# Optimization experiments

Hardware: AMD Instinct MI355X
Metric: run time of the kernel (lower is better)

The kernel has to match this reference:

```python
import jax, jax.numpy as jnp
import numpy as np

B, T, D, H = 4, 1024, 1024, 16


def setup_inputs() -> dict:
    key = jax.random.key(0)
    ks = jax.random.split(key, 8)
    s = 0.02
    return {
        "query": jax.random.normal(ks[0], (B, T, D), jnp.float32),
        "key": jax.random.normal(ks[1], (B, T, D), jnp.float32),
        "values": jax.random.normal(ks[2], (B, T, D), jnp.float32),
        "Wq": jax.random.normal(ks[3], (D, D), jnp.float32) * s,
        "bq": jnp.zeros((D,), jnp.float32),
        "Wv": jax.random.normal(ks[4], (D, D), jnp.float32) * s,
        "bv": jnp.zeros((D,), jnp.float32),
        "Wo": jax.random.normal(ks[5], (D, D), jnp.float32) * s,
        "bo": jnp.zeros((D,), jnp.float32),
        "gammas": jax.random.normal(ks[6], (H,), jnp.float32) * 0.1,
        "ln_g": jnp.ones((D,), jnp.float32),
        "ln_b": jnp.zeros((D,), jnp.float32),
    }


def _layer(query, key, values, Wq, bq, Wv, bv, Wo, bo, gammas, ln_g, ln_b):
    b, t, d = query.shape
    h = gammas.shape[0]
    dk = d // h

    def proj(x, W, bias):  # torch Linear: x @ W.T + b, then split heads -> (b,h,t,dk)
        y = jnp.einsum('btd,ed->bte', x, W) + bias
        return y.reshape(b, t, h, dk).transpose(0, 2, 1, 3)

    q = proj(query, Wq, bq)
    k = proj(key, Wq, bq)   # kq_same=True
    v = proj(values, Wv, bv)

    scores = jnp.einsum('bhqd,bhkd->bhqk', q, k) / np.float32(np.sqrt(dk))
    idx = jnp.arange(t)
    pos = jnp.abs(idx[:, None] - idx[None, :]).astype(scores.dtype)  # |i-j|, (t,t)
    mask = idx[:, None] > idx[None, :]  # strict lower tril (peek_cur=False)
    neg = jnp.asarray(-1e32, scores.dtype)

    # gamma time-effect (computed without grad in original)
    s_ = jax.nn.softmax(jnp.where(mask, scores, neg), axis=-1)
    distcum = jnp.cumsum(s_, axis=-1)
    disttotal = jnp.sum(s_, axis=-1, keepdims=True)
    dist = jnp.sqrt(jnp.clip((disttotal - distcum) * pos, 0.0, None))
    dist = jax.lax.stop_gradient(dist)
    gamma_eff = -jnp.abs(gammas)[None, :, None, None]  # (1,h,1,1)
    total_effect = jnp.clip(jnp.exp(dist * gamma_eff), 1e-5, 1e5)
    scores = scores * total_effect

    p = jax.nn.softmax(jnp.where(mask, scores, neg), axis=-1)
    p = jnp.where(mask, p, 0.0)
    # maxout rescale (maxout=True since peek_cur=False)
    scale = jnp.minimum(1.0 / jnp.max(p, axis=-1, keepdims=True), 5.0)
    p = p * scale

    out = jnp.einsum('bhqk,bhkd->bhqd', p, v)
    concat = out.transpose(0, 2, 1, 3).reshape(b, t, d)
    attn_out = jnp.einsum('btd,ed->bte', concat, Wo) + bo

    x = query + attn_out  # residual (dropout is identity in eval)
    mu = jnp.mean(x, axis=-1, keepdims=True)
    var = jnp.var(x, axis=-1, keepdims=True)
    return (x - mu) / jnp.sqrt(var + 1e-5) * ln_g + ln_b


def reference(query, key, values, Wq, bq, Wv, bv, Wo, bo, gammas, ln_g, ln_b):
    return _layer(query, key, values, Wq, bq, Wv, bv, Wo, bo, gammas, ln_g, ln_b)
```

## Files before the change

kernel.cpp:

```cpp
#include <hip/hip_runtime.h>
#include <hip/hip_bf16.h>
#include <stdint.h>


typedef unsigned short ushort_t;
typedef __attribute__((ext_vector_type(8))) short short8;
typedef __attribute__((ext_vector_type(8))) unsigned short u16x8;
typedef __attribute__((ext_vector_type(4))) float f32x4;
typedef __attribute__((ext_vector_type(4))) unsigned short u16x4;

#define GLB_CAST(p) ((const __attribute__((address_space(1))) void*)(p))
#define LDS_CAST(p) ((__attribute__((address_space(3))) void*)(p))

#if __has_builtin(__builtin_amdgcn_exp2f)
#define EXP2F(x) __builtin_amdgcn_exp2f(x)
#else
#define EXP2F(x) exp2f(x)
#endif

#define LOG2E 1.44269504f

__device__ __forceinline__ float b2f(ushort_t u) {
  union { unsigned int i; float f; } x; x.i = ((unsigned int)u) << 16; return x.f;
}
__device__ __forceinline__ ushort_t f2b(float f) {
  __hip_bfloat16 h = __float2bfloat16(f);
  return *reinterpret_cast<ushort_t*>(&h);
}
__device__ __forceinline__ float wave_sum(float v) {
  #pragma unroll
  for (int d = 32; d > 0; d >>= 1) v += __shfl_xor(v, d);
  return v;
}

__global__ void conv6_f32_bf16(const float* __restrict__ s0, const float* __restrict__ s1,
                               const float* __restrict__ s2, const float* __restrict__ s3,
                               const float* __restrict__ s4, const float* __restrict__ s5,
                               ushort_t* __restrict__ d0, ushort_t* __restrict__ d1,
                               ushort_t* __restrict__ d2, ushort_t* __restrict__ d3,
                               ushort_t* __restrict__ d4, ushort_t* __restrict__ d5,
                               int n4tok, int n4w) {
  const int y = blockIdx.y;
  const float* srcs[6] = {s0, s1, s2, s3, s4, s5};
  ushort_t*    dsts[6] = {d0, d1, d2, d3, d4, d5};
  const int n4 = (y < 3) ? n4tok : n4w;
  int i = blockIdx.x * blockDim.x + threadIdx.x;
  if (i < n4) {
    const float4 v = reinterpret_cast<const float4*>(srcs[y])[i];
    u16x4 o;
    o[0] = f2b(v.x); o[1] = f2b(v.y); o[2] = f2b(v.z); o[3] = f2b(v.w);
    reinterpret_cast<u16x4*>(dsts[y])[i] = o;
  }
}

__device__ __forceinline__ void gemm_core(const ushort_t* __restrict__ A,
                                          const ushort_t* __restrict__ Bt,
                                          int m0, int n0,
                                          ushort_t* As, ushort_t* Bs,
                                          f32x4 (&acc)[4][4]) {
  const int tid = threadIdx.x, lane = tid & 63;
  const int wid = tid >> 6;
  const int wr = (wid >> 1) * 64, wc = (wid & 1) * 64;
  for (int k0 = 0; k0 < 1024; k0 += 32) {
    #pragma unroll
    for (int it = 0; it < 2; ++it) {
      const int idx = tid * 8 + it * 2048;
      const int r = idx >> 5, kk = idx & 31;
      __builtin_amdgcn_global_load_lds(GLB_CAST(&A[(size_t)(m0 + r) * 1024 + k0 + kk]),
                                       LDS_CAST(&As[idx]), 16, 0, 0);
      __builtin_amdgcn_global_load_lds(GLB_CAST(&Bt[(size_t)(n0 + r) * 1024 + k0 + kk]),
                                       LDS_CAST(&Bs[idx]), 16, 0, 0);
    }
    __syncthreads();
    short8 af[4], bfv[4];
    #pragma unroll
    for (int m = 0; m < 4; ++m)
      af[m] = *reinterpret_cast<const short8*>(&As[(wr + m * 16 + (lane & 15)) * 32 + (lane >> 4) * 8]);
    #pragma unroll
    for (int n = 0; n < 4; ++n)
      bfv[n] = *reinterpret_cast<const short8*>(&Bs[(wc + n * 16 + (lane & 15)) * 32 + (lane >> 4) * 8]);
    #pragma unroll
    for (int m = 0; m < 4; ++m)
      #pragma unroll
      for (int n = 0; n < 4; ++n)
        acc[m][n] = __builtin_amdgcn_mfma_f32_16x16x32_bf16(af[m], bfv[n], acc[m][n], 0, 0, 0);
    __syncthreads();
  }
}

__global__ __launch_bounds__(256) void gemm_proj(
    const ushort_t* __restrict__ qb, const ushort_t* __restrict__ kb, const ushort_t* __restrict__ vb,
    const ushort_t* __restrict__ Wqb, const ushort_t* __restrict__ Wvb,
    const float* __restrict__ bq, const float* __restrict__ bvv,
    ushort_t* __restrict__ Qh, ushort_t* __restrict__ Kh, ushort_t* __restrict__ Vt) {
  __shared__ ushort_t As[128 * 32], Bs[128 * 32];
  const ushort_t* A; const ushort_t* Bt; const float* bias;
  if (blockIdx.z == 0)      { A = qb; Bt = Wqb; bias = bq;  }
  else if (blockIdx.z == 1) { A = kb; Bt = Wqb; bias = bq;  }
  else                      { A = vb; Bt = Wvb; bias = bvv; }
  const int m0 = blockIdx.y * 128, n0 = blockIdx.x * 128;
  f32x4 zero = {0.f, 0.f, 0.f, 0.f};
  f32x4 acc[4][4];
  #pragma unroll
  for (int m = 0; m < 4; ++m)
    #pragma unroll
    for (int n = 0; n < 4; ++n) acc[m][n] = zero;
  gemm_core(A, Bt, m0, n0, As, Bs, acc);
  const int lane = threadIdx.x & 63, wid = threadIdx.x >> 6;
  const int wr = (wid >> 1) * 64, wc = (wid & 1) * 64;
  if (blockIdx.z == 2) {
    #pragma unroll
    for (int m = 0; m < 4; ++m)
      #pragma unroll
      for (int n = 0; n < 4; ++n) {
        const int rowb = m0 + wr + m * 16 + (lane >> 4) * 4;
        const int col  = n0 + wc + n * 16 + (lane & 15);
        u16x4 pk;
        #pragma unroll
        for (int r4 = 0; r4 < 4; ++r4) pk[r4] = f2b(acc[m][n][r4] + bias[col]);
        const int bi = rowb >> 10, t = rowb & 1023;
        *reinterpret_cast<u16x4*>(
            &Vt[((size_t)(bi * 16 + (col >> 6)) * 64 + (col & 63)) * 1024 + t]) = pk;
      }
  } else {
    ushort_t* dst = (blockIdx.z == 0) ? Qh : Kh;
    #pragma unroll
    for (int m = 0; m < 4; ++m)
      #pragma unroll
      for (int n = 0; n < 4; ++n)
        #pragma unroll
        for (int r4 = 0; r4 < 4; ++r4) {
          const int row = m0 + wr + m * 16 + (lane >> 4) * 4 + r4;
          const int col = n0 + wc + n * 16 + (lane & 15);
          const float v = acc[m][n][r4] + bias[col];
          const int bi = row >> 10, t = row & 1023, h = col >> 6, dd = col & 63;
          dst[((size_t)(bi * 16 + h) * 1024 + t) * 64 + dd] = f2b(v);
        }
  }
}

__global__ __launch_bounds__(256) void gemm_out(
    const ushort_t* __restrict__ A, const ushort_t* __restrict__ Bt,
    const float* __restrict__ bias, const float* __restrict__ resid,
    float* __restrict__ dstF) {
  __shared__ ushort_t As[128 * 32], Bs[128 * 32];
  const int m0 = blockIdx.y * 128, n0 = blockIdx.x * 128;
  f32x4 zero = {0.f, 0.f, 0.f, 0.f};
  f32x4 acc[4][4];
  #pragma unroll
  for (int m = 0; m < 4; ++m)
    #pragma unroll
    for (int n = 0; n < 4; ++n) acc[m][n] = zero;
  gemm_core(A, Bt, m0, n0, As, Bs, acc);
  const int lane = threadIdx.x & 63, wid = threadIdx.x >> 6;
  const int wr = (wid >> 1) * 64, wc = (wid & 1) * 64;
  #pragma unroll
  for (int m = 0; m < 4; ++m)
    #pragma unroll
    for (int n = 0; n < 4; ++n)
      #pragma unroll
      for (int r4 = 0; r4 < 4; ++r4) {
        const int row = m0 + wr + m * 16 + (lane >> 4) * 4 + r4;
        const int col = n0 + wc + n * 16 + (lane & 15);
        const size_t o = (size_t)row * 1024 + col;
        dstF[o] = acc[m][n][r4] + bias[col] + resid[o];
      }
}

template<int CH>
__device__ __forceinline__ void phase_b(ushort_t* __restrict__ Sb, const int i0,
                                        const int w, const int lane, const float gamx) {
  const int c0 = CH * lane;
  int idxA = 0, idxB = 0;
  if constexpr (CH == 16) {
    const int ca = 2 * lane, cb = 2 * lane + 1;
    idxA = (ca ^ ((ca >> 3) & 7)) << 3;
    idxB = (cb ^ ((cb >> 3) & 7)) << 3;
  } else {
    const int c = c0 >> 3;
    idxA = ((c ^ ((c >> 3) & 7)) << 3) + (c0 & 7);
  }
  for (int rr = 0; rr < 4; ++rr) {
    const int r = w * 4 + rr;
    const int i = i0 + r;
    ushort_t* __restrict__ Row = &Sb[r * 1032];
    if (i == 0) {
      #pragma unroll
      for (int e = 0; e < CH; ++e) {
        if constexpr (CH == 16) Row[(e < 8) ? (idxA + e) : (idxB + e - 8)] = 0;
        else                    Row[idxA + e] = 0;
      }
      continue;
    }
    float s[CH];
    if constexpr (CH == 16) {
      const u16x8 ra = *reinterpret_cast<const u16x8*>(&Row[idxA]);
      const u16x8 rb = *reinterpret_cast<const u16x8*>(&Row[idxB]);
      #pragma unroll
      for (int e = 0; e < 8; ++e) { s[e] = b2f(ra[e]); s[8 + e] = b2f(rb[e]); }
    } else if constexpr (CH == 8) {
      const u16x8 ra = *reinterpret_cast<const u16x8*>(&Row[idxA]);
      #pragma unroll
      for (int e = 0; e < 8; ++e) s[e] = b2f(ra[e]);
    } else if constexpr (CH == 4) {
      const u16x4 ra = *reinterpret_cast<const u16x4*>(&Row[idxA]);
      #pragma unroll
      for (int e = 0; e < 4; ++e) s[e] = b2f(ra[e]);
    } else if constexpr (CH == 2) {
      s[0] = b2f(Row[idxA]); s[1] = b2f(Row[idxA + 1]);
    } else {
      s[0] = b2f(Row[idxA]);
    }
    const int nact = min(max(i - c0, 0), CH);
    float run = 0.f;
    #pragma unroll
    for (int e = 0; e < CH; ++e) {
      s[e] = (e < nact) ? s[e] * LOG2E : -__builtin_inff();
      run += EXP2F(s[e]);
    }
    float v = run;
    #pragma unroll
    for (int d = 1; d < 64; d <<= 1) {
      const float t = __shfl_down(v, d);
      v += (lane + d < 64) ? t : 0.f;
    }
    const float Z1 = __shfl(v, 0);
    const float excl = v - run;
    const float g2 = -gamx * rsqrtf(Z1);
    const float posb = (float)(i - c0);
    float run2 = excl;
    #pragma unroll
    for (int e = CH - 1; e >= 0; --e) {
      const float t = fmaxf(run2 * (posb - (float)e), 0.f);
      run2 += EXP2F(s[e]);
      const float eff = fmaxf(EXP2F(g2 * sqrtf(t)), 1e-5f);
      s[e] *= eff;
    }
    float z2 = 0.f, mm = 0.f;
    #pragma unroll
    for (int e = 0; e < CH; ++e) {
      const float p = EXP2F(s[e]);
      z2 += p;
      mm = fmaxf(mm, p);
    }
    #pragma unroll
    for (int d = 32; d > 0; d >>= 1) {
      z2 += __shfl_xor(z2, d);
      mm = fmaxf(mm, __shfl_xor(mm, d));
    }
    const float sc = fminf(1.f / mm, 5.f / z2);
    if constexpr (CH == 16) {
      u16x8 oa, ob;
      #pragma unroll
      for (int e = 0; e < 8; ++e) {
        oa[e] = f2b(EXP2F(s[e]) * sc);
        ob[e] = f2b(EXP2F(s[8 + e]) * sc);
      }
      *reinterpret_cast<u16x8*>(&Row[idxA]) = oa;
      *reinterpret_cast<u16x8*>(&Row[idxB]) = ob;
    } else if constexpr (CH == 8) {
      u16x8 oa;
      #pragma unroll
      for (int e = 0; e < 8; ++e) oa[e] = f2b(EXP2F(s[e]) * sc);
      *reinterpret_cast<u16x8*>(&Row[idxA]) = oa;
    } else if constexpr (CH == 4) {
      u16x4 oa;
      #pragma unroll
      for (int e = 0; e < 4; ++e) oa[e] = f2b(EXP2F(s[e]) * sc);
      *reinterpret_cast<u16x4*>(&Row[idxA]) = oa;
    } else if constexpr (CH == 2) {
      Row[idxA] = f2b(EXP2F(s[0]) * sc); Row[idxA + 1] = f2b(EXP2F(s[1]) * sc);
    } else {
      Row[idxA] = f2b(EXP2F(s[0]) * sc);
    }
  }
}

__global__ __launch_bounds__(256, 4) void attn_kernel(
    const ushort_t* __restrict__ Qh, const ushort_t* __restrict__ Kh,
    const ushort_t* __restrict__ Vt, const float* __restrict__ gammas,
    ushort_t* __restrict__ concat) {
  __shared__ __align__(16) ushort_t Sb[16 * 1032];
  __shared__ __align__(16) ushort_t Qs[16 * 72];
  const int tid = threadIdx.x, lane = tid & 63, w = tid >> 6;
  const int flat = blockIdx.x + (blockIdx.y << 6);
  const int bh = ((flat & 7) << 3) | (flat >> 9);
  const int i0 = ((flat >> 3) & 63) << 4;
  const int bi = bh >> 4, h = bh & 15;
  const size_t base = (size_t)bh * (1024 * 64);

  {
    const int r = tid >> 4, d = (tid & 15) * 4;
    *reinterpret_cast<u16x4*>(&Qs[r * 72 + d]) =
        *reinterpret_cast<const u16x4*>(&Qh[base + (size_t)(i0 + r) * 64 + d]);
  }
  __syncthreads();

  const int upper = i0 + 16;
  for (int nt = 0; nt < 16; ++nt) {
    const int colbase = (nt * 4 + w) * 16;
    if (colbase >= upper) break;
    f32x4 acc = {0.f, 0.f, 0.f, 0.f};
    #pragma unroll
    for (int kt = 0; kt < 2; ++kt) {
      const short8 a = *reinterpret_cast<const short8*>(
          &Qs[(lane & 15) * 72 + kt * 32 + (lane >> 4) * 8]);
      const short8 bb = *reinterpret_cast<const short8*>(
          &Kh[base + (size_t)(colbase + (lane & 15)) * 64 + kt * 32 + (lane >> 4) * 8]);
      acc = __builtin_amdgcn_mfma_f32_16x16x32_bf16(a, bb, acc, 0, 0, 0);
    }
    const int j = colbase + (lane & 15);
    const int cq = (j >> 3) ^ ((j >> 6) & 7);
    const int ub = cq * 8 + (j & 7);
    #pragma unroll
    for (int r4 = 0; r4 < 4; ++r4) {
      const int rf = (lane >> 4) * 4 + r4;
      Sb[rf * 1032 + ub] = f2b(acc[r4] * 0.125f);
    }
  }
  __syncthreads();

  const float gamx = fabsf(gammas[h]) * LOG2E;
  const int chp = (upper + 63) >> 6;
  if (chp == 1)      phase_b<1>(Sb, i0, w, lane, gamx);
  else if (chp == 2) phase_b<2>(Sb, i0, w, lane, gamx);
  else if (chp <= 4) phase_b<4>(Sb, i0, w, lane, gamx);
  else if (chp <= 8) phase_b<8>(Sb, i0, w, lane, gamx);
  else               phase_b<16>(Sb, i0, w, lane, gamx);
  __syncthreads();

  {
    const int d0 = w * 16;
    const int arow = lane & 15;
    const ushort_t* Prow = &Sb[arow * 1032];
    const ushort_t* Vrow = Vt + base + (size_t)(d0 + arow) * 1024;
    const int kmax = (upper + 31) & ~31;
    f32x4 acc = {0.f, 0.f, 0.f, 0.f};
    for (int k0 = 0; k0 < kmax; k0 += 32) {
      const int c = (k0 >> 3) + (lane >> 4);
      const int cq = c ^ ((c >> 3) & 7);
      const short8 a = *reinterpret_cast<const short8*>(&Prow[cq * 8]);
      const short8 bb = *reinterpret_cast<const short8*>(&Vrow[k0 + (lane >> 4) * 8]);
      acc = __builtin_amdgcn_mfma_f32_16x16x32_bf16(a, bb, acc, 0, 0, 0);
    }
    #pragma unroll
    for (int r4 = 0; r4 < 4; ++r4) {
      const int row = (lane >> 4) * 4 + r4;
      const int i = i0 + row;
      concat[((size_t)(bi * 1024 + i)) * 1024 + h * 64 + d0 + arow] = f2b(acc[r4]);
    }
  }
}

__global__ __launch_bounds__(256) void ln_kernel(const float* __restrict__ x,
                                                 const float* __restrict__ g,
                                                 const float* __restrict__ bb,
                                                 float* __restrict__ out) {
  const int row = blockIdx.x, tid = threadIdx.x, lane = tid & 63, w = tid >> 6;
  const float4 v = reinterpret_cast<const float4*>(x + (size_t)row * 1024)[tid];
  float s = v.x + v.y + v.z + v.w;
  float q = v.x * v.x + v.y * v.y + v.z * v.z + v.w * v.w;
  s = wave_sum(s); q = wave_sum(q);
  __shared__ float ps[4], pq[4];
  if (lane == 0) { ps[w] = s; pq[w] = q; }
  __syncthreads();
  const float ts = ps[0] + ps[1] + ps[2] + ps[3];
  const float tq = pq[0] + pq[1] + pq[2] + pq[3];
  const float mu = ts * (1.f / 1024.f);
  const float inv = rsqrtf(tq * (1.f / 1024.f) - mu * mu + 1e-5f);
  const float4 gv = reinterpret_cast<const float4*>(g)[tid];
  const float4 bv = reinterpret_cast<const float4*>(bb)[tid];
  float4 o;
  o.x = (v.x - mu) * inv * gv.x + bv.x;
  o.y = (v.y - mu) * inv * gv.y + bv.y;
  o.z = (v.z - mu) * inv * gv.z + bv.z;
  o.w = (v.w - mu) * inv * gv.w + bv.w;
  reinterpret_cast<float4*>(out + (size_t)row * 1024)[tid] = o;
}

extern "C" void kernel_launch(void* const* d_in, const int* in_sizes, int n_in,
                              void* d_out, int out_size, void* d_ws, size_t ws_size,
                              hipStream_t stream) {
  (void)in_sizes; (void)n_in; (void)out_size; (void)ws_size;
  const float* query  = (const float*)d_in[0];
  const float* key    = (const float*)d_in[1];
  const float* values = (const float*)d_in[2];
  const float* Wq     = (const float*)d_in[3];
  const float* bq     = (const float*)d_in[4];
  const float* Wv     = (const float*)d_in[5];
  const float* bv     = (const float*)d_in[6];
  const float* Wo     = (const float*)d_in[7];
  const float* bo     = (const float*)d_in[8];
  const float* gammas = (const float*)d_in[9];
  const float* ln_g   = (const float*)d_in[10];
  const float* ln_b   = (const float*)d_in[11];
  float* out = (float*)d_out;

  const size_t NT = 4096ull * 1024;
  const size_t NW = 1024ull * 1024;
  char* p = (char*)d_ws;
  ushort_t* qb  = (ushort_t*)p; p += NT * 2;
  ushort_t* kb  = (ushort_t*)p; p += NT * 2;
  ushort_t* vb  = (ushort_t*)p; p += NT * 2;
  ushort_t* Wqb = (ushort_t*)p; p += NW * 2;
  ushort_t* Wvb = (ushort_t*)p; p += NW * 2;
  ushort_t* Wob = (ushort_t*)p; p += NW * 2;
  ushort_t* Qh  = (ushort_t*)p; p += NT * 2;
  ushort_t* Kh  = (ushort_t*)p; p += NT * 2;
  ushort_t* Vt  = (ushort_t*)p; p += NT * 2;
  ushort_t* concat = vb;
  float*    xbuf   = (float*)qb;

  conv6_f32_bf16<<<dim3(4096, 6), 256, 0, stream>>>(
      query, key, values, Wq, Wv, Wo, qb, kb, vb, Wqb, Wvb, Wob,
      (int)(NT / 4), (int)(NW / 4));

  gemm_proj<<<dim3(8, 32, 3), 256, 0, stream>>>(qb, kb, vb, Wqb, Wvb, bq, bv, Qh, Kh, Vt);
  attn_kernel<<<dim3(64, 64), 256, 0, stream>>>(Qh, Kh, Vt, gammas, concat);
  gemm_out<<<dim3(8, 32), 256, 0, stream>>>(concat, Wob, bo, query, xbuf);
  ln_kernel<<<4096, 256, 0, stream>>>(xbuf, ln_g, ln_b, out);
}
```

Before: 181.0 us.

## Refine attention softmax phase: finer chunk sizes, cached exps, unswizzled LDS, reversed row order

Caches the first exp2 values and fuses the gamma-effect loop with the second softmax pass, so fewer exp2 calls run per element. Adds intermediate chunk-width instantiations (6, 10, 12, 14) so rows do less padded work. Drops the XOR swizzle on the score buffer in favour of plain contiguous indexing, and reverses the query-block order so the longest causal rows are scheduled first. The unswizzled layout may bring back LDS bank conflicts, and the odd chunk widths use narrower vector accesses, which may be misaligned for some widths.

After: 173.5 us. -4.1%, faster.

```diff
diff --git a/kernel.cpp b/kernel.cpp
--- a/kernel.cpp
+++ b/kernel.cpp
@@ -8,6 +8,7 @@
 typedef __attribute__((ext_vector_type(8))) unsigned short u16x8;
 typedef __attribute__((ext_vector_type(4))) float f32x4;
 typedef __attribute__((ext_vector_type(4))) unsigned short u16x4;
+typedef __attribute__((ext_vector_type(2))) unsigned short u16x2;
 
 #define GLB_CAST(p) ((const __attribute__((address_space(1))) void*)(p))
 #define LDS_CAST(p) ((__attribute__((address_space(3))) void*)(p))
@@ -168,55 +169,75 @@
 }
 
 template<int CH>
+__device__ __forceinline__ void load_row(const ushort_t* __restrict__ Row, float (&s)[CH]) {
+  constexpr int W = (CH % 8 == 0) ? 8 : (CH % 4 == 0) ? 4 : (CH % 2 == 0) ? 2 : 1;
+  #pragma unroll
+  for (int b = 0; b < CH / W; ++b) {
+    if constexpr (W == 8) {
+      const u16x8 t = *reinterpret_cast<const u16x8*>(&Row[b * 8]);
+      #pragma unroll
+      for (int e = 0; e < 8; ++e) s[b * 8 + e] = b2f(t[e]);
+    } else if constexpr (W == 4) {
+      const u16x4 t = *reinterpret_cast<const u16x4*>(&Row[b * 4]);
+      #pragma unroll
+      for (int e = 0; e < 4; ++e) s[b * 4 + e] = b2f(t[e]);
+    } else if constexpr (W == 2) {
+      const u16x2 t = *reinterpret_cast<const u16x2*>(&Row[b * 2]);
+      s[b * 2] = b2f(t[0]); s[b * 2 + 1] = b2f(t[1]);
+    } else {
+      s[b] = b2f(Row[b]);
+    }
+  }
+}
+
+template<int CH>
+__device__ __forceinline__ void store_row(ushort_t* __restrict__ Row,
+                                          const float (&p)[CH], const float sc) {
+  constexpr int W = (CH % 8 == 0) ? 8 : (CH % 4 == 0) ? 4 : (CH % 2 == 0) ? 2 : 1;
+  #pragma unroll
+  for (int b = 0; b < CH / W; ++b) {
+    if constexpr (W == 8) {
+      u16x8 o;
+      #pragma unroll
+      for (int e = 0; e < 8; ++e) o[e] = f2b(p[b * 8 + e] * sc);
+      *reinterpret_cast<u16x8*>(&Row[b * 8]) = o;
+    } else if constexpr (W == 4) {
+      u16x4 o;
+      #pragma unroll
+      for (int e = 0; e < 4; ++e) o[e] = f2b(p[b * 4 + e] * sc);
+      *reinterpret_cast<u16x4*>(&Row[b * 4]) = o;
+    } else if constexpr (W == 2) {
+      u16x2 o;
+      o[0] = f2b(p[b * 2] * sc); o[1] = f2b(p[b * 2 + 1] * sc);
+      *reinterpret_cast<u16x2*>(&Row[b * 2]) = o;
+    } else {
+      Row[b] = f2b(p[b] * sc);
+    }
+  }
+}
+
+template<int CH>
 __device__ __forceinline__ void phase_b(ushort_t* __restrict__ Sb, const int i0,
                                         const int w, const int lane, const float gamx) {
   const int c0 = CH * lane;
-  int idxA = 0, idxB = 0;
-  if constexpr (CH == 16) {
-    const int ca = 2 * lane, cb = 2 * lane + 1;
-    idxA = (ca ^ ((ca >> 3) & 7)) << 3;
-    idxB = (cb ^ ((cb >> 3) & 7)) << 3;
-  } else {
-    const int c = c0 >> 3;
-    idxA = ((c ^ ((c >> 3) & 7)) << 3) + (c0 & 7);
-  }
   for (int rr = 0; rr < 4; ++rr) {
     const int r = w * 4 + rr;
     const int i = i0 + r;
-    ushort_t* __restrict__ Row = &Sb[r * 1032];
+    ushort_t* __restrict__ Row = &Sb[r * 1032 + c0];
     if (i == 0) {
       #pragma unroll
-      for (int e = 0; e < CH; ++e) {
-        if constexpr (CH == 16) Row[(e < 8) ? (idxA + e) : (idxB + e - 8)] = 0;
-        else                    Row[idxA + e] = 0;
-      }
+      for (int e = 0; e < CH; ++e) Row[e] = 0;
       continue;
     }
-    float s[CH];
-    if constexpr (CH == 16) {
-      const u16x8 ra = *reinterpret_cast<const u16x8*>(&Row[idxA]);
-      const u16x8 rb = *reinterpret_cast<const u16x8*>(&Row[idxB]);
-      #pragma unroll
-      for (int e = 0; e < 8; ++e) { s[e] = b2f(ra[e]); s[8 + e] = b2f(rb[e]); }
-    } else if constexpr (CH == 8) {
-      const u16x8 ra = *reinterpret_cast<const u16x8*>(&Row[idxA]);
-      #pragma unroll
-      for (int e = 0; e < 8; ++e) s[e] = b2f(ra[e]);
-    } else if constexpr (CH == 4) {
-      const u16x4 ra = *reinterpret_cast<const u16x4*>(&Row[idxA]);
-      #pragma unroll
-      for (int e = 0; e < 4; ++e) s[e] = b2f(ra[e]);
-    } else if constexpr (CH == 2) {
-      s[0] = b2f(Row[idxA]); s[1] = b2f(Row[idxA + 1]);
-    } else {
-      s[0] = b2f(Row[idxA]);
-    }
     const int nact = min(max(i - c0, 0), CH);
+    float s[CH], ev[CH];
+    load_row<CH>(Row, s);
     float run = 0.f;
     #pragma unroll
     for (int e = 0; e < CH; ++e) {
       s[e] = (e < nact) ? s[e] * LOG2E : -__builtin_inff();
-      run += EXP2F(s[e]);
+      ev[e] = EXP2F(s[e]);
+      run += ev[e];
     }
     float v = run;
     #pragma unroll
@@ -225,21 +246,17 @@
       v += (lane + d < 64) ? t : 0.f;
     }
     const float Z1 = __shfl(v, 0);
-    const float excl = v - run;
+    float run2 = v - run;
     const float g2 = -gamx * rsqrtf(Z1);
     const float posb = (float)(i - c0);
-    float run2 = excl;
+    float z2 = 0.f, mm = 0.f;
     #pragma unroll
     for (int e = CH - 1; e >= 0; --e) {
       const float t = fmaxf(run2 * (posb - (float)e), 0.f);
-      run2 += EXP2F(s[e]);
+      run2 += ev[e];
       const float eff = fmaxf(EXP2F(g2 * sqrtf(t)), 1e-5f);
-      s[e] *= eff;
-    }
-    float z2 = 0.f, mm = 0.f;
-    #pragma unroll
-    for (int e = 0; e < CH; ++e) {
-      const float p = EXP2F(s[e]);
+      const float p = EXP2F(s[e] * eff);
+      ev[e] = p;
       z2 += p;
       mm = fmaxf(mm, p);
     }
@@ -249,30 +266,7 @@
       mm = fmaxf(mm, __shfl_xor(mm, d));
     }
     const float sc = fminf(1.f / mm, 5.f / z2);
-    if constexpr (CH == 16) {
-      u16x8 oa, ob;
-      #pragma unroll
-      for (int e = 0; e < 8; ++e) {
-        oa[e] = f2b(EXP2F(s[e]) * sc);
-        ob[e] = f2b(EXP2F(s[8 + e]) * sc);
-      }
-      *reinterpret_cast<u16x8*>(&Row[idxA]) = oa;
-      *reinterpret_cast<u16x8*>(&Row[idxB]) = ob;
-    } else if constexpr (CH == 8) {
-      u16x8 oa;
-      #pragma unroll
-      for (int e = 0; e < 8; ++e) oa[e] = f2b(EXP2F(s[e]) * sc);
-      *reinterpret_cast<u16x8*>(&Row[idxA]) = oa;
-    } else if constexpr (CH == 4) {
-      u16x4 oa;
-      #pragma unroll
-      for (int e = 0; e < 4; ++e) oa[e] = f2b(EXP2F(s[e]) * sc);
-      *reinterpret_cast<u16x4*>(&Row[idxA]) = oa;
-    } else if constexpr (CH == 2) {
-      Row[idxA] = f2b(EXP2F(s[0]) * sc); Row[idxA + 1] = f2b(EXP2F(s[1]) * sc);
-    } else {
-      Row[idxA] = f2b(EXP2F(s[0]) * sc);
-    }
+    store_row<CH>(Row, ev, sc);
   }
 }
 
@@ -285,7 +279,7 @@
   const int tid = threadIdx.x, lane = tid & 63, w = tid >> 6;
   const int flat = blockIdx.x + (blockIdx.y << 6);
   const int bh = ((flat & 7) << 3) | (flat >> 9);
-  const int i0 = ((flat >> 3) & 63) << 4;
+  const int i0 = (63 - ((flat >> 3) & 63)) << 4;
   const int bi = bh >> 4, h = bh & 15;
   const size_t base = (size_t)bh * (1024 * 64);
 
@@ -310,23 +304,27 @@
       acc = __builtin_amdgcn_mfma_f32_16x16x32_bf16(a, bb, acc, 0, 0, 0);
     }
     const int j = colbase + (lane & 15);
-    const int cq = (j >> 3) ^ ((j >> 6) & 7);
-    const int ub = cq * 8 + (j & 7);
     #pragma unroll
     for (int r4 = 0; r4 < 4; ++r4) {
       const int rf = (lane >> 4) * 4 + r4;
-      Sb[rf * 1032 + ub] = f2b(acc[r4] * 0.125f);
+      Sb[rf * 1032 + j] = f2b(acc[r4] * 0.125f);
     }
   }
   __syncthreads();
 
   const float gamx = fabsf(gammas[h]) * LOG2E;
   const int chp = (upper + 63) >> 6;
-  if (chp == 1)      phase_b<1>(Sb, i0, w, lane, gamx);
-  else if (chp == 2) phase_b<2>(Sb, i0, w, lane, gamx);
-  else if (chp <= 4) phase_b<4>(Sb, i0, w, lane, gamx);
-  else if (chp <= 8) phase_b<8>(Sb, i0, w, lane, gamx);
-  else               phase_b<16>(Sb, i0, w, lane, gamx);
+  switch (chp) {
+    case 1:           phase_b<1 >(Sb, i0, w, lane, gamx); break;
+    case 2:           phase_b<2 >(Sb, i0, w, lane, gamx); break;
+    case 3: case 4:   phase_b<4 >(Sb, i0, w, lane, gamx); break;
+    case 5: case 6:   phase_b<6 >(Sb, i0, w, lane, gamx); break;
+    case 7: case 8:   phase_b<8 >(Sb, i0, w, lane, gamx); break;
+    case 9: case 10:  phase_b<10>(Sb, i0, w, lane, gamx); break;
+    case 11: case 12: phase_b<12>(Sb, i0, w, lane, gamx); break;
+    case 13: case 14: phase_b<14>(Sb, i0, w, lane, gamx); break;
+    default:          phase_b<16>(Sb, i0, w, lane, gamx); break;
+  }
   __syncthreads();
 
   {
@@ -337,9 +335,7 @@
     const int kmax = (upper + 31) & ~31;
     f32x4 acc = {0.f, 0.f, 0.f, 0.f};
     for (int k0 = 0; k0 < kmax; k0 += 32) {
-      const int c = (k0 >> 3) + (lane >> 4);
-      const int cq = c ^ ((c >> 3) & 7);
-      const short8 a = *reinterpret_cast<const short8*>(&Prow[cq * 8]);
+      const short8 a = *reinterpret_cast<const short8*>(&Prow[k0 + (lane >> 4) * 8]);
       const short8 bb = *reinterpret_cast<const short8*>(&Vrow[k0 + (lane >> 4) * 8]);
       acc = __builtin_amdgcn_mfma_f32_16x16x32_bf16(a, bb, acc, 0, 0, 0);
     }
```
